# Kernel optimization log

Hardware: AMD Instinct MI355X
Metric: run time of the kernel (lower is better)

Reference implementation:

```python
import jax, jax.numpy as jnp
import numpy as np

B, S, H = 2, 1024, 2048
E_ROUTED = 8
E = E_ROUTED + 1          # +1 unconditional expert
I_MOE = 1408
I_SHARED = 5632
TOP_K = 2
UNCOND_LABEL = 1000
EPS = 1e-12


def setup_inputs() -> dict:
    key = jax.random.key(0)
    ks = jax.random.split(key, 9)
    hidden_states = jax.random.normal(ks[0], (B, S, H), dtype=jnp.float32)
    labels = jax.random.randint(ks[1], (B,), 0, 1001)
    labels = labels.at[0].set(UNCOND_LABEL)  # ensure uncond path is exercised
    cluster_centers = 0.02 * jax.random.normal(ks[2], (E_ROUTED, H), dtype=jnp.float32)
    sc = 0.02
    Wg = sc * jax.random.normal(ks[3], (E, H, I_MOE), dtype=jnp.float32)
    Wu = sc * jax.random.normal(ks[4], (E, H, I_MOE), dtype=jnp.float32)
    Wd = sc * jax.random.normal(ks[5], (E, I_MOE, H), dtype=jnp.float32)
    Wg_s = sc * jax.random.normal(ks[6], (H, I_SHARED), dtype=jnp.float32)
    Wu_s = sc * jax.random.normal(ks[7], (H, I_SHARED), dtype=jnp.float32)
    Wd_s = sc * jax.random.normal(ks[8], (I_SHARED, H), dtype=jnp.float32)
    return {"hidden_states": hidden_states, "labels": labels,
            "cluster_centers": cluster_centers,
            "Wg": Wg, "Wu": Wu, "Wd": Wd,
            "Wg_s": Wg_s, "Wu_s": Wu_s, "Wd_s": Wd_s}


def _l2norm(x):
    return x / jnp.sqrt(jnp.sum(x * x, axis=-1, keepdims=True) + EPS)


def reference(hidden_states, labels, cluster_centers, Wg, Wu, Wd, Wg_s, Wu_s, Wd_s):
    b, s, h = hidden_states.shape
    x = hidden_states.reshape(-1, h)                       # [T, H]
    flat_labels = jnp.repeat(labels, s)                     # [T]
    uncond = flat_labels == UNCOND_LABEL                    # [T]

    # cosine-sim router over routed experts
    cos = _l2norm(x) @ _l2norm(cluster_centers).T           # [T, E_routed]
    probs = jax.nn.softmax(cos, axis=-1)
    top_v, top_i = jax.lax.top_k(probs, TOP_K)              # [T, K]

    # uncond tokens: weight 1.0 in slot 0, all slots -> uncond expert (E-1)
    uncond_w = jnp.concatenate(
        [jnp.ones((1,), jnp.float32), jnp.zeros((TOP_K - 1,), jnp.float32)])
    weights = jnp.where(uncond[:, None], uncond_w[None, :], top_v)   # [T, K]
    indices = jnp.where(uncond[:, None], E - 1, top_i)               # [T, K]

    # combine weights per (token, expert): sum of slot weights hitting expert e
    onehot = (indices[:, :, None] == jnp.arange(E)[None, None, :])   # [T, K, E]
    cw = jnp.sum(weights[:, :, None] * onehot, axis=1)               # [T, E]

    # grouped expert MLPs (dense over experts; zero combine weight masks out)
    g = jnp.einsum('th,ehi->tei', x, Wg)
    u = jnp.einsum('th,ehi->tei', x, Wu)
    eo = jnp.einsum('tei,eih->teh', jax.nn.silu(g) * u, Wd)          # [T, E, H]
    out = jnp.einsum('teh,te->th', eo, cw)                           # [T, H]

    # shared expert on all tokens
    shared = (jax.nn.silu(x @ Wg_s) * (x @ Wu_s)) @ Wd_s             # [T, H]

    return (out + shared).reshape(b, s, h)
```

## Files before the change

kernel.cpp:

```cpp
#include <hip/hip_runtime.h>
#include <hip/hip_bf16.h>
#include <stdint.h>

#define T_TOK 2048
#define H_DIM 2048
#define S_SEQ 1024
#define NE_ROUTED 8
#define NE 9
#define IMOE 1408
#define ISHARED 5632
#define UNCOND_LBL 1000

typedef short bf16x8 __attribute__((ext_vector_type(8)));
typedef float f32x4 __attribute__((ext_vector_type(4)));

__device__ __forceinline__ unsigned short f2bf(float f) {
  union { float f; unsigned int u; } v; v.f = f;
  unsigned int u = v.u;
  return (unsigned short)((u + 0x7fffu + ((u >> 16) & 1u)) >> 16);
}

__device__ __forceinline__ void gl16(const void* g, void* l) {
  __builtin_amdgcn_global_load_lds(
      (const __attribute__((address_space(1))) unsigned int*)g,
      (__attribute__((address_space(3))) unsigned int*)l, 16, 0, 0);
}

__global__ __launch_bounds__(256) void cvt_bf16_kernel(const float* __restrict__ in,
                                                       unsigned short* __restrict__ out,
                                                       int n) {
  int i = (blockIdx.x * 256 + threadIdx.x) * 4;
  if (i >= n) return;
  float4 v = *(const float4*)(in + i);
  uint2 p;
  p.x = (unsigned)f2bf(v.x) | ((unsigned)f2bf(v.y) << 16);
  p.y = (unsigned)f2bf(v.z) | ((unsigned)f2bf(v.w) << 16);
  *(uint2*)(out + i) = p;
}

__global__ __launch_bounds__(256) void router_kernel(
    const float* __restrict__ x, const int* __restrict__ labels,
    const float* __restrict__ cc,
    int* __restrict__ counts, int* __restrict__ toklist, float* __restrict__ wts) {
  int t = (int)((blockIdx.x * 256 + threadIdx.x) >> 6);
  int lane = threadIdx.x & 63;
  if (t >= T_TOK) return;
  const float* xp = x + (size_t)t * H_DIM;
  float xx = 0.f;
  float d[NE_ROUTED], cn[NE_ROUTED];
#pragma unroll
  for (int e = 0; e < NE_ROUTED; e++) { d[e] = 0.f; cn[e] = 0.f; }
  for (int h = lane; h < H_DIM; h += 64) {
    float xv = xp[h];
    xx += xv * xv;
#pragma unroll
    for (int e = 0; e < NE_ROUTED; e++) {
      float cv = cc[e * H_DIM + h];
      d[e] += xv * cv;
      cn[e] += cv * cv;
    }
  }
#pragma unroll
  for (int off = 32; off > 0; off >>= 1) {
    xx += __shfl_xor(xx, off);
#pragma unroll
    for (int e = 0; e < NE_ROUTED; e++) {
      d[e] += __shfl_xor(d[e], off);
      cn[e] += __shfl_xor(cn[e], off);
    }
  }
  if (lane == 0) {
    int lab = labels[t / S_SEQ];
    if (lab == UNCOND_LBL) {
      int r = atomicAdd(&counts[NE - 1], 1);
      toklist[(NE - 1) * T_TOK + r] = t;
      wts[(NE - 1) * T_TOK + r] = 1.0f;
    } else {
      float xn = sqrtf(xx + 1e-12f);
      float cosv[NE_ROUTED];
      float mx = -1e30f;
#pragma unroll
      for (int e = 0; e < NE_ROUTED; e++) {
        cosv[e] = d[e] / (xn * sqrtf(cn[e] + 1e-12f));
        mx = fmaxf(mx, cosv[e]);
      }
      float p[NE_ROUTED];
      float s = 0.f;
#pragma unroll
      for (int e = 0; e < NE_ROUTED; e++) { p[e] = __expf(cosv[e] - mx); s += p[e]; }
      int i1 = 0;
#pragma unroll
      for (int e = 1; e < NE_ROUTED; e++) if (p[e] > p[i1]) i1 = e;
      int i2 = (i1 == 0) ? 1 : 0;
#pragma unroll
      for (int e = 0; e < NE_ROUTED; e++) if (e != i2 && e != i1 && p[e] > p[i2]) i2 = e;
      int r1 = atomicAdd(&counts[i1], 1);
      toklist[i1 * T_TOK + r1] = t;
      wts[i1 * T_TOK + r1] = p[i1] / s;
      int r2 = atomicAdd(&counts[i2], 1);
      toklist[i2 * T_TOK + r2] = t;
      wts[i2 * T_TOK + r2] = p[i2] / s;
    }
  }
}

__global__ __launch_bounds__(256) void build_desc(
    const int* __restrict__ counts, int* __restrict__ desc,
    int* __restrict__ descd, int* __restrict__ nact) {
  int tid = threadIdx.x;
  for (int i = tid; i < 352; i += 256) {
    int nt = i >> 3, mt = i & 7;
    desc[i] = (1 << 30) | (nt << 8) | mt;
  }
  int off[NE + 1];
  off[0] = 352;
  for (int e = 0; e < NE; e++) {
    int c = counts[e];
    int mtmax = (c + 255) >> 8;
    if (mtmax > 8) mtmax = 8;
    off[e + 1] = off[e] + mtmax * 11;
  }
  for (int e = 0; e < NE; e++) {
    int base = off[e];
    int n = off[e + 1] - base;
    if (n == 0) continue;
    int mtmax = n / 11;
    for (int i = tid; i < n; i += 256) {
      int nt = i / mtmax, mt = i % mtmax;
      desc[base + i] = (e << 16) | (nt << 8) | mt;
    }
  }
  if (tid == 0) nact[0] = off[NE];
  for (int i = tid; i < 128; i += 256) {
    int nt = i >> 3, mt = i & 7;
    descd[i] = (1 << 30) | (nt << 8) | mt;
  }
  int offd[NE + 1];
  offd[0] = 128;
  for (int e = 0; e < NE; e++) {
    int c = counts[e];
    int mtmax = (c + 255) >> 8;
    if (mtmax > 8) mtmax = 8;
    offd[e + 1] = offd[e] + mtmax * 16;
  }
  for (int e = 0; e < NE; e++) {
    int base = offd[e];
    int n = offd[e + 1] - base;
    if (n == 0) continue;
    int mtmax = n / 16;
    for (int i = tid; i < n; i += 256) {
      int nt = i / mtmax, mt = i % mtmax;
      descd[base + i] = (e << 16) | (nt << 8) | mt;
    }
  }
  if (tid == 0) nact[1] = offd[NE] - 128;
}


__device__ __forceinline__ void transpose_body(
    const float* __restrict__ src, unsigned short* __restrict__ dst,
    int K, int N, int e, int kt, int n0, int t) {
  int NS = N >> 4, KT = K >> 5;
  const float* sp0 = src + (size_t)e * K * N + (size_t)kt * 32 * N + n0;
  __shared__ float tile[32][72];
  int kr = t >> 3, nc = (t & 7) << 3;
  const float* sp = sp0 + (size_t)kr * N + nc;
  float4 a = *(const float4*)sp;
  float4 b = *(const float4*)(sp + 4);
  *(float4*)&tile[kr][nc] = a;
  *(float4*)&tile[kr][nc + 4] = b;
  __syncthreads();
  int nsl = t >> 6, up = t & 63;
  int ul = up ^ ((up >> 3) & 7);
  int rn = ul >> 2, fq = ul & 3;
  int nl = (nsl << 4) + rn;
  unsigned int pk[4];
#pragma unroll
  for (int j = 0; j < 4; j++) {
    float f0 = tile[fq * 8 + 2 * j][nl];
    float f1 = tile[fq * 8 + 2 * j + 1][nl];
    pk[j] = (unsigned)f2bf(f0) | ((unsigned)f2bf(f1) << 16);
  }
  size_t ns = (size_t)e * NS + (n0 >> 4) + nsl;
  unsigned short* dp = dst + (ns * KT + kt) * 512 + up * 8;
  *(uint4*)dp = make_uint4(pk[0], pk[1], pk[2], pk[3]);
}

__global__ __launch_bounds__(256) void transpose_all(
    const float* __restrict__ Wg, const float* __restrict__ Wu,
    const float* __restrict__ Wd, const float* __restrict__ Wgs,
    const float* __restrict__ Wus, const float* __restrict__ Wds,
    unsigned short* __restrict__ WgT, unsigned short* __restrict__ WuT,
    unsigned short* __restrict__ WdT, unsigned short* __restrict__ WgsT,
    unsigned short* __restrict__ WusT, unsigned short* __restrict__ WdsT) {
  int lid = blockIdx.x;
  int t = threadIdx.x;
  if (lid < 12672) {
    int e = lid / 1408, r = lid % 1408;
    int kt = r / 22, n0 = (r % 22) << 6;
    transpose_body(Wg, WgT, H_DIM, IMOE, e, kt, n0, t);
  } else if (lid < 25344) {
    int r0 = lid - 12672;
    int e = r0 / 1408, r = r0 % 1408;
    int kt = r / 22, n0 = (r % 22) << 6;
    transpose_body(Wu, WuT, H_DIM, IMOE, e, kt, n0, t);
  } else if (lid < 38016) {
    int r0 = lid - 25344;
    int e = r0 / 1408, r = r0 % 1408;
    int kt = r / 32, n0 = (r % 32) << 6;
    transpose_body(Wd, WdT, IMOE, H_DIM, e, kt, n0, t);
  } else if (lid < 43648) {
    int r = lid - 38016;
    int kt = r / 88, n0 = (r % 88) << 6;
    transpose_body(Wgs, WgsT, H_DIM, ISHARED, 0, kt, n0, t);
  } else if (lid < 49280) {
    int r = lid - 43648;
    int kt = r / 88, n0 = (r % 88) << 6;
    transpose_body(Wus, WusT, H_DIM, ISHARED, 0, kt, n0, t);
  } else {
    int r = lid - 49280;
    int kt = r / 32, n0 = (r % 32) << 6;
    transpose_body(Wds, WdsT, ISHARED, H_DIM, 0, kt, n0, t);
  }
}

__global__ __launch_bounds__(1024) void up_merged(
    const unsigned short* __restrict__ X,
    const unsigned short* __restrict__ WgT, const unsigned short* __restrict__ WuT,
    const unsigned short* __restrict__ WgsT, const unsigned short* __restrict__ WusT,
    unsigned short* __restrict__ HhT, unsigned short* __restrict__ HsT,
    const int* __restrict__ toklist, const int* __restrict__ counts,
    const int* __restrict__ desc, const int* __restrict__ nact) {
  const int KT = 64;
  int d = blockIdx.x;
  int nv = nact[0];
  int q = nv >> 3, r = nv & 7;
  int x = d & 7, j = d >> 3;
  int cap = q + (x < r ? 1 : 0);
  if (j >= cap) return;
  int idx = (x < r ? x * (q + 1) : r * (q + 1) + (x - r) * q) + j;
  int dv = desc[idx];
  bool sh = (dv >> 30) != 0;
  int e = (dv >> 16) & 0xff;
  int nt = (dv >> 8) & 0xff;
  int mt = dv & 0xff;

  int cnt = sh ? T_TOK : counts[e];
  int m0 = mt * 256;
  if (m0 >= cnt) return;
  int n0 = nt * 128;
  int NS = sh ? (ISHARED >> 4) : (IMOE >> 4);
  int KTO = sh ? (ISHARED >> 5) : (IMOE >> 5);
  unsigned short* Hout = sh ? HsT : HhT;
  size_t hb = sh ? 0 : (size_t)e * (T_TOK >> 4);

  __shared__ unsigned short As[4][8192];
  __shared__ unsigned short Bgs[4][4096];
  __shared__ unsigned short Bus[4][4096];

  int tid = threadIdx.x, lane = tid & 63, wid = tid >> 6;
  int wm = wid >> 2, wn = wid & 3;
  int fr = lane & 15, fq = lane >> 4;

  int v = lane ^ ((lane >> 3) & 7);
  int rr = m0 + wid * 16 + (v >> 2);
  if (rr >= cnt) rr = cnt - 1;
  int tok = sh ? rr : toklist[e * T_TOK + rr];
  const unsigned short* aptr = X + (size_t)tok * H_DIM + ((v & 3) << 3);

  size_t nsg = (sh ? 0 : (size_t)e * NS) + (n0 >> 4) + (wid & 7);
  const unsigned short* bsrc =
      ((wid >> 3) ? (sh ? WusT : WuT) : (sh ? WgsT : WgT)) + nsg * KT * 512 + lane * 8;
  unsigned short* bdstBase = (wid >> 3) ? &Bus[0][0] : &Bgs[0][0];

  int fo = fr * 4 + fq;
  fo = (fo ^ ((fo >> 3) & 7)) * 8;

  f32x4 zero = {0.f, 0.f, 0.f, 0.f};
  f32x4 accg[4][2], accu[4][2];
#pragma unroll
  for (int i = 0; i < 4; i++)
#pragma unroll
    for (int jj = 0; jj < 2; jj++) { accg[i][jj] = zero; accu[i][jj] = zero; }

  auto stageA = [&](int b, int t) {
    gl16(aptr + (size_t)t * 32, &As[b][wid * 512]);
  };
  auto stageB = [&](int b, int t) {
    gl16(bsrc + (size_t)t * 512, bdstBase + b * 4096 + (wid & 7) * 512);
  };

  stageA(0, 0); stageB(0, 0);
  stageA(1, 1); stageB(1, 1);
  stageA(2, 2); stageB(2, 2);
  asm volatile("s_waitcnt vmcnt(4)" ::: "memory");
  __builtin_amdgcn_s_barrier();

  for (int t = 0; t < KT; ++t) {
    int b = t & 3;
    bf16x8 af[4], bgf[2];
#pragma unroll
    for (int mi = 0; mi < 4; mi++)
      af[mi] = *(const bf16x8*)&As[b][(wm * 4 + mi) * 512 + fo];
#pragma unroll
    for (int ni = 0; ni < 2; ni++)
      bgf[ni] = *(const bf16x8*)&Bgs[b][(wn * 2 + ni) * 512 + fo];
    if (t + 3 < KT) stageA((t + 3) & 3, t + 3);
    __builtin_amdgcn_s_setprio(1);
#pragma unroll
    for (int mi = 0; mi < 4; mi++)
#pragma unroll
      for (int ni = 0; ni < 2; ni++)
        accg[mi][ni] = __builtin_amdgcn_mfma_f32_16x16x32_bf16(af[mi], bgf[ni], accg[mi][ni], 0, 0, 0);
    __builtin_amdgcn_s_setprio(0);
    bf16x8 buf2[2];
#pragma unroll
    for (int ni = 0; ni < 2; ni++)
      buf2[ni] = *(const bf16x8*)&Bus[b][(wn * 2 + ni) * 512 + fo];
    if (t + 3 < KT) stageB((t + 3) & 3, t + 3);
    __builtin_amdgcn_s_setprio(1);
#pragma unroll
    for (int mi = 0; mi < 4; mi++)
#pragma unroll
      for (int ni = 0; ni < 2; ni++)
        accu[mi][ni] = __builtin_amdgcn_mfma_f32_16x16x32_bf16(af[mi], buf2[ni], accu[mi][ni], 0, 0, 0);
    __builtin_amdgcn_s_setprio(0);
    if (t + 3 < KT) {
      asm volatile("s_waitcnt vmcnt(4)" ::: "memory");
      __builtin_amdgcn_s_barrier();
    } else if (t + 2 < KT) {
      asm volatile("s_waitcnt vmcnt(2)" ::: "memory");
      __builtin_amdgcn_s_barrier();
    } else if (t + 1 < KT) {
      asm volatile("s_waitcnt vmcnt(0)" ::: "memory");
      __builtin_amdgcn_s_barrier();
    }
  }

#pragma unroll
  for (int mi = 0; mi < 4; mi++) {
    int rb = m0 + wm * 64 + mi * 16;
    if (rb >= cnt) continue;
    int ms = rb >> 4;
#pragma unroll
    for (int ni = 0; ni < 2; ni++) {
      int col = n0 + wn * 32 + ni * 16 + fr;
      int kto = col >> 5;
      int c3 = (col >> 3) & 3;
      int jcol = col & 7;
      size_t base = ((hb + ms) * (size_t)KTO + kto) * 512 + jcol;
#pragma unroll
      for (int jj = 0; jj < 4; jj++) {
        int row = rb + fq * 4 + jj;
        if (row < cnt) {
          float g = accg[mi][ni][jj];
          float u = accu[mi][ni][jj];
          float h = g / (1.f + __expf(-g)) * u;
          int ul = (fq * 4 + jj) * 4 + c3;
          int ph = ul ^ ((ul >> 3) & 7);
          Hout[base + ph * 8] = f2bf(h);
        }
      }
    }
  }
}

__global__ __launch_bounds__(1024) void down_merged(
    const unsigned short* __restrict__ HhT, const unsigned short* __restrict__ HsT,
    const unsigned short* __restrict__ WdT, const unsigned short* __restrict__ WdsT,
    float* __restrict__ Out,
    const int* __restrict__ toklist, const float* __restrict__ wts,
    const int* __restrict__ counts,
    const int* __restrict__ descd, const int* __restrict__ nact) {
  int d = blockIdx.x;
  int x = d & 7, j = d >> 3;
  int dv;
  if (j < 16) {
    dv = descd[x * 16 + j];
  } else {
    int R = nact[1];
    int jr = j - 16;
    int q = R >> 3, r = R & 7;
    int cap = q + (x < r ? 1 : 0);
    if (jr >= cap) return;
    int idx = (x < r ? x * (q + 1) : r * (q + 1) + (x - r) * q) + jr;
    dv = descd[128 + idx];
  }
  bool sh = (dv >> 30) != 0;
  int e = (dv >> 16) & 0xff;
  int nt = (dv >> 8) & 0xff;
  int mt = dv & 0xff;

  int cnt = sh ? T_TOK : counts[e];
  int m0 = mt * 256;
  if (m0 >= cnt) return;
  int n0 = nt * 128;
  int KT = sh ? (ISHARED >> 5) : (IMOE >> 5);
  const int NS = H_DIM >> 4;

  __shared__ unsigned short As[4][8192];
  __shared__ unsigned short Bs[4][4096];

  int tid = threadIdx.x, lane = tid & 63, wid = tid >> 6;
  int wm = wid >> 2, wn = wid & 3;
  int fr = lane & 15, fq = lane >> 4;

  const unsigned short* Hin = sh ? HsT : HhT;
  size_t mbase = sh ? 0 : (size_t)e * (T_TOK >> 4);
  size_t ms = mbase + (m0 >> 4) + wid;
  const unsigned short* ap = Hin + ms * KT * 512 + lane * 8;
  size_t nsg = (sh ? 0 : (size_t)e * NS) + (n0 >> 4) + (wid & 7);
  const unsigned short* bp = (sh ? WdsT : WdT) + nsg * KT * 512 + lane * 8;

  int fo = fr * 4 + fq;
  fo = (fo ^ ((fo >> 3) & 7)) * 8;

  f32x4 zero = {0.f, 0.f, 0.f, 0.f};
  f32x4 acc[4][2];
#pragma unroll
  for (int i = 0; i < 4; i++)
#pragma unroll
    for (int jj = 0; jj < 2; jj++) acc[i][jj] = zero;

  bool hasB = (wid < 8);
  auto stage = [&](int b, int t) {
    gl16(ap + (size_t)t * 512, &As[b][wid * 512]);
    if (hasB) gl16(bp + (size_t)t * 512, &Bs[b][(wid & 7) * 512]);
  };

  stage(0, 0);
  stage(1, 1);
  stage(2, 2);
  if (hasB) { asm volatile("s_waitcnt vmcnt(4)" ::: "memory"); }
  else      { asm volatile("s_waitcnt vmcnt(2)" ::: "memory"); }
  __builtin_amdgcn_s_barrier();

  for (int t = 0; t < KT; ++t) {
    int b = t & 3;
    bf16x8 af[4], bf[2];
#pragma unroll
    for (int mi = 0; mi < 4; mi++)
      af[mi] = *(const bf16x8*)&As[b][(wm * 4 + mi) * 512 + fo];
#pragma unroll
    for (int ni = 0; ni < 2; ni++)
      bf[ni] = *(const bf16x8*)&Bs[b][(wn * 2 + ni) * 512 + fo];
    if (t + 3 < KT) stage((t + 3) & 3, t + 3);
    __builtin_amdgcn_s_setprio(1);
#pragma unroll
    for (int mi = 0; mi < 4; mi++)
#pragma unroll
      for (int ni = 0; ni < 2; ni++)
        acc[mi][ni] = __builtin_amdgcn_mfma_f32_16x16x32_bf16(af[mi], bf[ni], acc[mi][ni], 0, 0, 0);
    __builtin_amdgcn_s_setprio(0);
    if (t + 3 < KT) {
      if (hasB) { asm volatile("s_waitcnt vmcnt(4)" ::: "memory"); }
      else      { asm volatile("s_waitcnt vmcnt(2)" ::: "memory"); }
      __builtin_amdgcn_s_barrier();
    } else if (t + 2 < KT) {
      if (hasB) { asm volatile("s_waitcnt vmcnt(2)" ::: "memory"); }
      else      { asm volatile("s_waitcnt vmcnt(1)" ::: "memory"); }
      __builtin_amdgcn_s_barrier();
    } else if (t + 1 < KT) {
      asm volatile("s_waitcnt vmcnt(0)" ::: "memory");
      __builtin_amdgcn_s_barrier();
    }
  }

  int rbase = m0 + wm * 64;
  int cbase = n0 + wn * 32;
#pragma unroll
  for (int mi = 0; mi < 4; mi++)
#pragma unroll
    for (int ni = 0; ni < 2; ni++) {
      int col = cbase + ni * 16 + fr;
#pragma unroll
      for (int jj = 0; jj < 4; jj++) {
        int row = rbase + mi * 16 + fq * 4 + jj;
        if (row < cnt) {
          float vv = acc[mi][ni][jj];
          int tk;
          float wgt;
          if (sh) { tk = row; wgt = 1.0f; }
          else { tk = toklist[e * T_TOK + row]; wgt = wts[e * T_TOK + row]; }
          atomicAdd(&Out[(size_t)tk * H_DIM + col], wgt * vv);
        }
      }
    }
}

extern "C" void kernel_launch(void* const* d_in, const int* in_sizes, int n_in,
                              void* d_out, int out_size, void* d_ws, size_t ws_size,
                              hipStream_t stream) {
  const float* x = (const float*)d_in[0];
  const int* labels = (const int*)d_in[1];
  const float* cc = (const float*)d_in[2];
  const float* Wg = (const float*)d_in[3];
  const float* Wu = (const float*)d_in[4];
  const float* Wd = (const float*)d_in[5];
  const float* Wgs = (const float*)d_in[6];
  const float* Wus = (const float*)d_in[7];
  const float* Wds = (const float*)d_in[8];
  float* out = (float*)d_out;

  uint8_t* p = (uint8_t*)d_ws;
  int* counts = (int*)p;            p += 256;
  int* desc = (int*)p;              p += 1152 * 4;
  int* descd = (int*)p;             p += 1344 * 4;
  int* nact = (int*)p;              p += 256;
  int* toklist = (int*)p;           p += (size_t)NE * T_TOK * 4;
  float* wts = (float*)p;           p += (size_t)NE * T_TOK * 4;
  unsigned short* xbf = (unsigned short*)p;  p += (size_t)T_TOK * H_DIM * 2;
  unsigned short* WgT = (unsigned short*)p;  p += (size_t)NE * H_DIM * IMOE * 2;
  unsigned short* WuT = (unsigned short*)p;  p += (size_t)NE * H_DIM * IMOE * 2;
  unsigned short* WdT = (unsigned short*)p;  p += (size_t)NE * IMOE * H_DIM * 2;
  unsigned short* WgsT = (unsigned short*)p; p += (size_t)H_DIM * ISHARED * 2;
  unsigned short* WusT = (unsigned short*)p; p += (size_t)H_DIM * ISHARED * 2;
  unsigned short* WdsT = (unsigned short*)p; p += (size_t)ISHARED * H_DIM * 2;
  unsigned short* HhT = (unsigned short*)p;  p += (size_t)NE * T_TOK * IMOE * 2;
  unsigned short* HsT = (unsigned short*)p;  p += (size_t)T_TOK * ISHARED * 2;
  size_t need = (size_t)(p - (uint8_t*)d_ws);
  if (ws_size < need) return;

  hipMemsetAsync(d_ws, 0, 64, stream);
  hipMemsetAsync(d_out, 0, (size_t)out_size * 4, stream);
  cvt_bf16_kernel<<<(T_TOK * H_DIM / 4 + 255) / 256, 256, 0, stream>>>(x, xbf, T_TOK * H_DIM);
  router_kernel<<<T_TOK / 4, 256, 0, stream>>>(x, labels, cc, counts, toklist, wts);
  build_desc<<<1, 256, 0, stream>>>(counts, desc, descd, nact);

  transpose_all<<<54912, 256, 0, stream>>>(Wg, Wu, Wd, Wgs, Wus, Wds,
                                           WgT, WuT, WdT, WgsT, WusT, WdsT);

  up_merged<<<1144, 1024, 0, stream>>>(xbf, WgT, WuT, WgsT, WusT, HhT, HsT,
                                       toklist, counts, desc, nact);

  down_merged<<<1280, 1024, 0, stream>>>(HhT, HsT, WdT, WdsT, out,
                                         toklist, wts, counts, descd, nact);
}
```

Before: 485.2 us.

## Widen down-projection N tile to 256 and split shared-expert K in two

The down-projection GEMM now computes 256x256 output tiles instead of 256x128. Every wave loads B fragments, and each wave runs a 4x4 MFMA accumulator grid. This halves how often the A (hidden activation) tiles are re-read across N and doubles the MFMA work per LDS fragment load. To keep enough blocks for the large shared expert, its K dimension is split into two chunks encoded in the descriptor; both chunks accumulate through the existing atomicAdd epilogue. In exchange, LDS use per block doubles to 128KB, register pressure rises, atomic traffic on the output increases for the shared expert, and the grid shrinks to 704 blocks, which may reduce occupancy and load balance.

```diff
diff --git a/kernel.cpp b/kernel.cpp
--- a/kernel.cpp
+++ b/kernel.cpp
@@ -132,8 +132,11 @@
   }
   if (tid == 0) nact[0] = off[NE];
   for (int i = tid; i < 128; i += 256) {
-    int nt = i >> 3, mt = i & 7;
-    descd[i] = (1 << 30) | (nt << 8) | mt;
+    int x = i >> 4, j = i & 15;
+    int nt = x;
+    int mt = j >> 1;
+    int kc = j & 1;
+    descd[i] = (1 << 30) | (kc << 28) | (nt << 8) | mt;
   }
   int offd[NE + 1];
   offd[0] = 128;
@@ -141,13 +144,13 @@
     int c = counts[e];
     int mtmax = (c + 255) >> 8;
     if (mtmax > 8) mtmax = 8;
-    offd[e + 1] = offd[e] + mtmax * 16;
+    offd[e + 1] = offd[e] + mtmax * 8;
   }
   for (int e = 0; e < NE; e++) {
     int base = offd[e];
     int n = offd[e + 1] - base;
     if (n == 0) continue;
-    int mtmax = n / 16;
+    int mtmax = n / 8;
     for (int i = tid; i < n; i += 256) {
       int nt = i / mtmax, mt = i % mtmax;
       descd[base + i] = (e << 16) | (nt << 8) | mt;
@@ -387,6 +390,7 @@
     dv = descd[128 + idx];
   }
   bool sh = (dv >> 30) != 0;
+  int kc = (dv >> 28) & 3;
   int e = (dv >> 16) & 0xff;
   int nt = (dv >> 8) & 0xff;
   int mt = dv & 0xff;
@@ -394,12 +398,14 @@
   int cnt = sh ? T_TOK : counts[e];
   int m0 = mt * 256;
   if (m0 >= cnt) return;
-  int n0 = nt * 128;
-  int KT = sh ? (ISHARED >> 5) : (IMOE >> 5);
+  int n0 = nt * 256;
+  int KTfull = sh ? (ISHARED >> 5) : (IMOE >> 5);
+  int KT = sh ? 88 : 44;
+  int koff = kc * 88;
   const int NS = H_DIM >> 4;
 
   __shared__ unsigned short As[4][8192];
-  __shared__ unsigned short Bs[4][4096];
+  __shared__ unsigned short Bs[4][8192];
 
   int tid = threadIdx.x, lane = tid & 63, wid = tid >> 6;
   int wm = wid >> 2, wn = wid & 3;
@@ -408,57 +414,53 @@
   const unsigned short* Hin = sh ? HsT : HhT;
   size_t mbase = sh ? 0 : (size_t)e * (T_TOK >> 4);
   size_t ms = mbase + (m0 >> 4) + wid;
-  const unsigned short* ap = Hin + ms * KT * 512 + lane * 8;
-  size_t nsg = (sh ? 0 : (size_t)e * NS) + (n0 >> 4) + (wid & 7);
-  const unsigned short* bp = (sh ? WdsT : WdT) + nsg * KT * 512 + lane * 8;
+  const unsigned short* ap = Hin + ms * (size_t)KTfull * 512 + lane * 8;
+  size_t nsg = (sh ? 0 : (size_t)e * NS) + (n0 >> 4) + wid;
+  const unsigned short* bp = (sh ? WdsT : WdT) + nsg * (size_t)KTfull * 512 + lane * 8;
 
   int fo = fr * 4 + fq;
   fo = (fo ^ ((fo >> 3) & 7)) * 8;
 
   f32x4 zero = {0.f, 0.f, 0.f, 0.f};
-  f32x4 acc[4][2];
+  f32x4 acc[4][4];
 #pragma unroll
   for (int i = 0; i < 4; i++)
 #pragma unroll
-    for (int jj = 0; jj < 2; jj++) acc[i][jj] = zero;
-
-  bool hasB = (wid < 8);
+    for (int jj = 0; jj < 4; jj++) acc[i][jj] = zero;
+
   auto stage = [&](int b, int t) {
-    gl16(ap + (size_t)t * 512, &As[b][wid * 512]);
-    if (hasB) gl16(bp + (size_t)t * 512, &Bs[b][(wid & 7) * 512]);
+    gl16(ap + (size_t)(koff + t) * 512, &As[b][wid * 512]);
+    gl16(bp + (size_t)(koff + t) * 512, &Bs[b][wid * 512]);
   };
 
   stage(0, 0);
   stage(1, 1);
   stage(2, 2);
-  if (hasB) { asm volatile("s_waitcnt vmcnt(4)" ::: "memory"); }
-  else      { asm volatile("s_waitcnt vmcnt(2)" ::: "memory"); }
+  asm volatile("s_waitcnt vmcnt(4)" ::: "memory");
   __builtin_amdgcn_s_barrier();
 
   for (int t = 0; t < KT; ++t) {
     int b = t & 3;
-    bf16x8 af[4], bf[2];
+    bf16x8 af[4], bf[4];
 #pragma unroll
     for (int mi = 0; mi < 4; mi++)
       af[mi] = *(const bf16x8*)&As[b][(wm * 4 + mi) * 512 + fo];
 #pragma unroll
-    for (int ni = 0; ni < 2; ni++)
-      bf[ni] = *(const bf16x8*)&Bs[b][(wn * 2 + ni) * 512 + fo];
+    for (int ni = 0; ni < 4; ni++)
+      bf[ni] = *(const bf16x8*)&Bs[b][(wn * 4 + ni) * 512 + fo];
     if (t + 3 < KT) stage((t + 3) & 3, t + 3);
     __builtin_amdgcn_s_setprio(1);
 #pragma unroll
     for (int mi = 0; mi < 4; mi++)
 #pragma unroll
-      for (int ni = 0; ni < 2; ni++)
+      for (int ni = 0; ni < 4; ni++)
         acc[mi][ni] = __builtin_amdgcn_mfma_f32_16x16x32_bf16(af[mi], bf[ni], acc[mi][ni], 0, 0, 0);
     __builtin_amdgcn_s_setprio(0);
     if (t + 3 < KT) {
-      if (hasB) { asm volatile("s_waitcnt vmcnt(4)" ::: "memory"); }
-      else      { asm volatile("s_waitcnt vmcnt(2)" ::: "memory"); }
+      asm volatile("s_waitcnt vmcnt(4)" ::: "memory");
       __builtin_amdgcn_s_barrier();
     } else if (t + 2 < KT) {
-      if (hasB) { asm volatile("s_waitcnt vmcnt(2)" ::: "memory"); }
-      else      { asm volatile("s_waitcnt vmcnt(1)" ::: "memory"); }
+      asm volatile("s_waitcnt vmcnt(2)" ::: "memory");
       __builtin_amdgcn_s_barrier();
     } else if (t + 1 < KT) {
       asm volatile("s_waitcnt vmcnt(0)" ::: "memory");
@@ -467,11 +469,11 @@
   }
 
   int rbase = m0 + wm * 64;
-  int cbase = n0 + wn * 32;
+  int cbase = n0 + wn * 64;
 #pragma unroll
   for (int mi = 0; mi < 4; mi++)
 #pragma unroll
-    for (int ni = 0; ni < 2; ni++) {
+    for (int ni = 0; ni < 4; ni++) {
       int col = cbase + ni * 16 + fr;
 #pragma unroll
       for (int jj = 0; jj < 4; jj++) {
@@ -533,6 +535,6 @@
   up_merged<<<1144, 1024, 0, stream>>>(xbf, WgT, WuT, WgsT, WusT, HhT, HsT,
                                        toklist, counts, desc, nact);
 
-  down_merged<<<1280, 1024, 0, stream>>>(HhT, HsT, WdT, WdsT, out,
-                                         toklist, wts, counts, descd, nact);
-}
+  down_merged<<<704, 1024, 0, stream>>>(HhT, HsT, WdT, WdsT, out,
+                                        toklist, wts, counts, descd, nact);
+}
```

Result: faster. 472.4 us (-2.6%).
